# Performance work log

Hardware: AMD Instinct MI355X
Metric: run time of the kernel (lower is better)

Reference implementation:

```python
import jax, jax.numpy as jnp
import numpy as np

B, T, C = 2, 2048, 1024
NH, HS = 16, 64  # n_heads, head_size; NH*HS == C


def setup_inputs() -> dict:
    key = jax.random.key(0)
    k1, k2, k3 = jax.random.split(key, 3)
    x = jax.random.normal(k1, (B, T, C), dtype=jnp.float32)
    W_attn = jax.random.normal(k2, (C, 3 * C), dtype=jnp.float32) * (C ** -0.5)
    b_attn = jax.random.normal(k3, (3 * C,), dtype=jnp.float32) * 0.02
    return {"x": x, "W_attn": W_attn, "b_attn": b_attn}


def reference(x, W_attn, b_attn):
    Bv, Tv, Cv = x.shape
    qkv = x @ W_attn + b_attn                       # [B,T,3C]
    q, k, v = jnp.split(qkv, 3, axis=-1)            # each [B,T,C]
    q = q.reshape(Bv, Tv, NH, HS)
    k = k.reshape(Bv, Tv, NH, HS)
    v = v.reshape(Bv, Tv, NH, HS)
    scale = HS ** -0.5
    wei = jnp.einsum('bqhd,bkhd->bhqk', q, k) * scale  # [B,H,T,T]
    causal = jnp.tril(jnp.ones((Tv, Tv), dtype=bool))
    wei = jnp.where(causal[None, None], wei, -jnp.inf)
    wei = jax.nn.softmax(wei, axis=-1)
    # dropout layers are identity in eval mode
    out = jnp.einsum('bhqk,bkhd->bqhd', wei, v)     # [B,T,H,HS]
    return out.reshape(Bv, Tv, Cv)
```

## Files before the change

### kernel.cpp

```cpp
#include <hip/hip_runtime.h>
#include <hip/hip_bf16.h>
#include <math.h>

#define BB   2
#define TT   2048
#define CC   1024
#define NH   16
#define HS   64
#define N3C  3072
#define MM   4096

typedef __attribute__((ext_vector_type(8))) short bf16x8;
typedef __attribute__((ext_vector_type(4))) float f32x4;

#define NINF (-__builtin_inff())
#define QSCALE 0.125f

__device__ __forceinline__ unsigned short f2bf(float f) {
    unsigned int u = __builtin_bit_cast(unsigned int, f);
    unsigned int r = u + 0x7fffu + ((u >> 16) & 1u);
    return (unsigned short)(r >> 16);
}

__device__ __forceinline__ unsigned short f2bf_fast(float f) {
    unsigned int u = __builtin_bit_cast(unsigned int, f);
    return (unsigned short)((u + 0x8000u) >> 16);
}

__device__ __forceinline__ void gl_lds16(const unsigned short* g, unsigned short* l) {
    __builtin_amdgcn_global_load_lds(
        (const __attribute__((address_space(1))) unsigned int*)g,
        (__attribute__((address_space(3))) unsigned int*)l, 16, 0, 0);
}

__global__ __launch_bounds__(256) void k_cast(const float* __restrict__ x,
                                              unsigned short* __restrict__ xb) {
    int i = (blockIdx.x * 256 + threadIdx.x) * 4;
    float4 v = *(const float4*)(x + i);
    ushort4 o;
    o.x = f2bf(v.x); o.y = f2bf(v.y); o.z = f2bf(v.z); o.w = f2bf(v.w);
    *(ushort4*)(xb + i) = o;
}

__global__ __launch_bounds__(256) void k_transpose_w(const float* __restrict__ W,
                                                     unsigned short* __restrict__ Wt) {
    __shared__ float tile[32][33];
    const int n0 = blockIdx.x * 32;
    const int k0 = blockIdx.y * 32;
    const int t = threadIdx.x;
    {
        int kr = t >> 3, ns = (t & 7) * 4;
        float4 v = *(const float4*)(W + (size_t)(k0 + kr) * N3C + n0 + ns);
        tile[kr][ns + 0] = v.x; tile[kr][ns + 1] = v.y;
        tile[kr][ns + 2] = v.z; tile[kr][ns + 3] = v.w;
    }
    __syncthreads();
    {
        int nr = t >> 3, ks = (t & 7) * 4;
        ushort4 o;
        o.x = f2bf(tile[ks + 0][nr]);
        o.y = f2bf(tile[ks + 1][nr]);
        o.z = f2bf(tile[ks + 2][nr]);
        o.w = f2bf(tile[ks + 3][nr]);
        *(ushort4*)(Wt + (size_t)(n0 + nr) * CC + k0 + ks) = o;
    }
}

#define EPS 72

__global__ __launch_bounds__(256) void k_gemm_qkv(const unsigned short* __restrict__ xb,
                                                  const unsigned short* __restrict__ wt,
                                                  const float* __restrict__ bias,
                                                  unsigned short* __restrict__ qb,
                                                  unsigned short* __restrict__ kb,
                                                  unsigned short* __restrict__ vt) {
    __shared__ unsigned short sA[128 * 32];
    __shared__ unsigned short sB[128 * 32];
    __shared__ unsigned short sE[4 * 64 * EPS];
    const int t = threadIdx.x;
    const int wave = t >> 6, lane = t & 63;
    const int quad = lane >> 4, c16 = lane & 15;
    const int wm = wave >> 1, wn = wave & 1;
    const int m0 = blockIdx.y * 128;
    const int n0 = blockIdx.x * 128;
    const int sel = n0 >> 10;

    f32x4 acc[4][4];
#pragma unroll
    for (int i = 0; i < 4; ++i)
#pragma unroll
        for (int j = 0; j < 4; ++j) acc[i][j] = f32x4{0, 0, 0, 0};

    const int srow = wave * 16 + (lane >> 2);
    const int scol = (lane & 3) * 8;
    const unsigned short* gA = xb + (size_t)(m0 + srow) * CC + scol;
    const unsigned short* gB = wt + (size_t)(n0 + srow) * CC + scol;
    unsigned short* lA = sA + wave * 512 + lane * 8;
    unsigned short* lB = sB + wave * 512 + lane * 8;

    for (int k0 = 0; k0 < CC; k0 += 32) {
        __syncthreads();
        gl_lds16(gA + k0, lA);
        gl_lds16(gA + k0 + (size_t)64 * CC, lA + 2048);
        gl_lds16(gB + k0, lB);
        gl_lds16(gB + k0 + (size_t)64 * CC, lB + 2048);
        __syncthreads();
        bf16x8 a[4], b[4];
#pragma unroll
        for (int rt = 0; rt < 4; ++rt)
            a[rt] = *(const bf16x8*)(sA + (wm * 64 + rt * 16 + c16) * 32 + quad * 8);
#pragma unroll
        for (int ct = 0; ct < 4; ++ct)
            b[ct] = *(const bf16x8*)(sB + (wn * 64 + ct * 16 + c16) * 32 + quad * 8);
#pragma unroll
        for (int rt = 0; rt < 4; ++rt)
#pragma unroll
            for (int ct = 0; ct < 4; ++ct)
                acc[rt][ct] = __builtin_amdgcn_mfma_f32_16x16x32_bf16(b[ct], a[rt], acc[rt][ct], 0, 0, 0);
    }

    const int head = ((n0 + wn * 64) >> 6) & 15;
    const int bh = (m0 >> 11) * NH + head;
    const int tbase = (m0 & 2047) + wm * 64;
    if (sel < 2) {
        unsigned short* dst = (sel == 0) ? qb : kb;
        const float sc = (sel == 0) ? QSCALE : 1.0f;
        unsigned short* ew = sE + wave * (64 * EPS);
#pragma unroll
        for (int ct = 0; ct < 4; ++ct) {
            const float4 bv4 = *(const float4*)(bias + n0 + wn * 64 + ct * 16 + quad * 4);
            const int d0 = ct * 16 + quad * 4;
#pragma unroll
            for (int rt = 0; rt < 4; ++rt) {
                ushort4 pk;
                pk.x = f2bf((acc[rt][ct][0] + bv4.x) * sc);
                pk.y = f2bf((acc[rt][ct][1] + bv4.y) * sc);
                pk.z = f2bf((acc[rt][ct][2] + bv4.z) * sc);
                pk.w = f2bf((acc[rt][ct][3] + bv4.w) * sc);
                *(ushort4*)(ew + (rt * 16 + c16) * EPS + d0) = pk;
            }
        }
        const size_t gbase = ((size_t)bh * TT + tbase) * HS;
#pragma unroll
        for (int i = 0; i < 8; ++i) {
            const int trow = i * 8 + (lane >> 3);
            bf16x8 row = *(const bf16x8*)(ew + trow * EPS + (lane & 7) * 8);
            *(bf16x8*)(dst + gbase + (size_t)trow * HS + (lane & 7) * 8) = row;
        }
    } else {
#pragma unroll
        for (int ct = 0; ct < 4; ++ct) {
            const float4 bv4 = *(const float4*)(bias + n0 + wn * 64 + ct * 16 + quad * 4);
#pragma unroll
            for (int r = 0; r < 4; ++r) {
                const int d = ct * 16 + quad * 4 + r;
                const float bv = ((const float*)&bv4)[r];
#pragma unroll
                for (int rt = 0; rt < 4; ++rt) {
                    const int tt = tbase + rt * 16 + c16;
                    vt[((size_t)bh * HS + d) * TT + tt] = f2bf(acc[rt][ct][r] + bv);
                }
            }
        }
    }
}

#define SPP 72
#define AW  4

__global__ __launch_bounds__(256) void k_attn(const unsigned short* __restrict__ qb,
                                              const unsigned short* __restrict__ kb,
                                              const unsigned short* __restrict__ vt,
                                              float* __restrict__ out) {
    __shared__ unsigned short sK[2][64 * 64];
    __shared__ unsigned short sV[2][64 * 64];
    __shared__ unsigned short sP[AW][32 * SPP];

    const int tid = threadIdx.x;
    const int wave = tid >> 6, lane = tid & 63;
    const int quad = lane >> 4, c16 = lane & 15;
    const int g = blockIdx.x >> 5;
    const int qbk = 15 - g;
    const int bh = blockIdx.x & 31;
    const int qw = qbk * 128 + wave * 32;
    const int qmax = qw + 31;
    const int kiters = 2 * (qbk + 1);

    const unsigned short* Qp = qb + (size_t)bh * TT * HS;
    const unsigned short* Kp = kb + (size_t)bh * TT * HS;
    const unsigned short* Vp = vt + (size_t)bh * HS * TT;

    bf16x8 qf[2][2];
#pragma unroll
    for (int j = 0; j < 2; ++j)
#pragma unroll
        for (int ks = 0; ks < 2; ++ks)
            qf[j][ks] = *(const bf16x8*)(Qp + (size_t)(qw + j * 16 + c16) * HS + ks * 32 + quad * 8);

    f32x4 o[4][2];
#pragma unroll
    for (int dt = 0; dt < 4; ++dt)
#pragma unroll
        for (int j = 0; j < 2; ++j) o[dt][j] = f32x4{0, 0, 0, 0};
    float lsum[2] = {0.f, 0.f};

    unsigned short* sPw = sP[wave];

    const int srow = tid >> 3;
    const int ssc = tid & 7;
    auto stage = [&](int buf, int kt) {
        const int kb0 = kt * 64;
#pragma unroll
        for (int rnd = 0; rnd < 2; ++rnd) {
            const int row = rnd * 32 + srow;
            const int sl = ((ssc ^ (row & 7)) * 8);
            gl_lds16(Kp + (size_t)(kb0 + row) * HS + sl, &sK[buf][rnd * 2048 + tid * 8]);
            gl_lds16(Vp + (size_t)row * TT + kb0 + sl, &sV[buf][rnd * 2048 + tid * 8]);
        }
    };

    auto tile = [&](int buf, int kt) {
        const int kb0 = kt * 64;
        const unsigned short* Kb = sK[buf];
        const unsigned short* Vb = sV[buf];
        bf16x8 kf[4][2];
#pragma unroll
        for (int mt = 0; mt < 4; ++mt)
#pragma unroll
            for (int ks = 0; ks < 2; ++ks)
                kf[mt][ks] = *(const bf16x8*)(Kb + (mt * 16 + c16) * 64 +
                                              (((ks * 4 + quad) ^ (c16 & 7)) * 8));
        f32x4 s[4][2];
#pragma unroll
        for (int mt = 0; mt < 4; ++mt)
#pragma unroll
            for (int j = 0; j < 2; ++j) s[mt][j] = f32x4{0, 0, 0, 0};
#pragma unroll
        for (int mt = 0; mt < 4; ++mt)
#pragma unroll
            for (int j = 0; j < 2; ++j) {
                s[mt][j] = __builtin_amdgcn_mfma_f32_16x16x32_bf16(kf[mt][0], qf[j][0], s[mt][j], 0, 0, 0);
                s[mt][j] = __builtin_amdgcn_mfma_f32_16x16x32_bf16(kf[mt][1], qf[j][1], s[mt][j], 0, 0, 0);
            }
        bf16x8 vf[4][2];
#pragma unroll
        for (int dt = 0; dt < 4; ++dt)
#pragma unroll
            for (int ks = 0; ks < 2; ++ks)
                vf[dt][ks] = *(const bf16x8*)(Vb + (dt * 16 + c16) * 64 +
                                              (((ks * 4 + quad) ^ (c16 & 7)) * 8));
        const bool maskit = (kb0 + 63 > qw);
#pragma unroll
        for (int j = 0; j < 2; ++j) {
            const int rowq = qw + j * 16 + c16;
            float l = 0.f;
#pragma unroll
            for (int mt = 0; mt < 4; ++mt) {
                float p0, p1, p2, p3;
                if (maskit) {
                    const int k = kb0 + mt * 16 + quad * 4;
                    p0 = __expf((k     <= rowq) ? s[mt][j][0] : NINF);
                    p1 = __expf((k + 1 <= rowq) ? s[mt][j][1] : NINF);
                    p2 = __expf((k + 2 <= rowq) ? s[mt][j][2] : NINF);
                    p3 = __expf((k + 3 <= rowq) ? s[mt][j][3] : NINF);
                } else {
                    p0 = __expf(s[mt][j][0]);
                    p1 = __expf(s[mt][j][1]);
                    p2 = __expf(s[mt][j][2]);
                    p3 = __expf(s[mt][j][3]);
                }
                l += (p0 + p1) + (p2 + p3);
                ushort4 pk;
                pk.x = f2bf_fast(p0); pk.y = f2bf_fast(p1);
                pk.z = f2bf_fast(p2); pk.w = f2bf_fast(p3);
                *(ushort4*)(sPw + (j * 16 + c16) * SPP + mt * 16 + quad * 4) = pk;
            }
            lsum[j] += l;
        }
        bf16x8 pf[2][2];
#pragma unroll
        for (int j = 0; j < 2; ++j)
#pragma unroll
            for (int ks = 0; ks < 2; ++ks)
                pf[j][ks] = *(const bf16x8*)(sPw + (j * 16 + c16) * SPP + ks * 32 + quad * 8);
#pragma unroll
        for (int dt = 0; dt < 4; ++dt)
#pragma unroll
            for (int j = 0; j < 2; ++j) {
                o[dt][j] = __builtin_amdgcn_mfma_f32_16x16x32_bf16(vf[dt][0], pf[j][0], o[dt][j], 0, 0, 0);
                o[dt][j] = __builtin_amdgcn_mfma_f32_16x16x32_bf16(vf[dt][1], pf[j][1], o[dt][j], 0, 0, 0);
            }
    };

    stage(0, 0);
    for (int kt = 0; kt < kiters; ++kt) {
        if (kt + 1 < kiters) {
            stage((kt + 1) & 1, kt + 1);
            asm volatile("s_waitcnt vmcnt(4)" ::: "memory");
        } else {
            asm volatile("s_waitcnt vmcnt(0)" ::: "memory");
        }
        __builtin_amdgcn_s_barrier();
        asm volatile("" ::: "memory");
        if (kt * 64 <= qmax) tile(kt & 1, kt);
        __builtin_amdgcn_s_barrier();
        asm volatile("" ::: "memory");
    }

#pragma unroll
    for (int j = 0; j < 2; ++j) {
        lsum[j] += __shfl_xor(lsum[j], 16);
        lsum[j] += __shfl_xor(lsum[j], 32);
    }

    const int b_ = bh >> 4, h_ = bh & 15;
#pragma unroll
    for (int j = 0; j < 2; ++j) {
        const float il = 1.0f / lsum[j];
        const int q = qw + j * 16 + c16;
        float* orow = out + ((size_t)(b_ * TT + q)) * CC + h_ * HS;
#pragma unroll
        for (int dt = 0; dt < 4; ++dt) {
            float4 w;
            w.x = o[dt][j][0] * il; w.y = o[dt][j][1] * il;
            w.z = o[dt][j][2] * il; w.w = o[dt][j][3] * il;
            *(float4*)(orow + dt * 16 + quad * 4) = w;
        }
    }
}

extern "C" void kernel_launch(void* const* d_in, const int* in_sizes, int n_in,
                              void* d_out, int out_size, void* d_ws, size_t ws_size,
                              hipStream_t stream) {
    const float* x    = (const float*)d_in[0];
    const float* W    = (const float*)d_in[1];
    const float* bias = (const float*)d_in[2];
    float* out = (float*)d_out;

    char* ws = (char*)d_ws;
    unsigned short* xb = (unsigned short*)(ws);
    unsigned short* wt = (unsigned short*)(ws + 8388608);
    unsigned short* qb = (unsigned short*)(ws + 8388608 + 6291456);
    unsigned short* kb = (unsigned short*)(ws + 8388608 + 6291456 + 8388608);
    unsigned short* vt = (unsigned short*)(ws + 8388608 + 6291456 + 2 * 8388608);

    k_cast<<<dim3(MM * CC / (256 * 4)), dim3(256), 0, stream>>>(x, xb);
    k_transpose_w<<<dim3(N3C / 32, CC / 32), dim3(256), 0, stream>>>(W, wt);
    k_gemm_qkv<<<dim3(N3C / 128, MM / 128), dim3(256), 0, stream>>>(xb, wt, bias, qb, kb, vt);
    k_attn<<<dim3(16 * 32), dim3(256), 0, stream>>>(qb, kb, vt, out);
}
```

Baseline: 179.2 us.

## Pair causal query blocks in attention, widen GEMM K-tile, stage V transpose via LDS

```diff
diff --git a/kernel.cpp b/kernel.cpp
--- a/kernel.cpp
+++ b/kernel.cpp
@@ -74,9 +74,11 @@
                                                   unsigned short* __restrict__ qb,
                                                   unsigned short* __restrict__ kb,
                                                   unsigned short* __restrict__ vt) {
-    __shared__ unsigned short sA[128 * 32];
-    __shared__ unsigned short sB[128 * 32];
-    __shared__ unsigned short sE[4 * 64 * EPS];
+    __shared__ unsigned short smem[4 * 64 * EPS];
+    unsigned short* sA = smem;
+    unsigned short* sB = smem + 128 * 64;
+    unsigned short* sE = smem;
+
     const int t = threadIdx.x;
     const int wave = t >> 6, lane = t & 63;
     const int quad = lane >> 4, c16 = lane & 15;
@@ -91,33 +93,38 @@
 #pragma unroll
         for (int j = 0; j < 4; ++j) acc[i][j] = f32x4{0, 0, 0, 0};
 
-    const int srow = wave * 16 + (lane >> 2);
-    const int scol = (lane & 3) * 8;
-    const unsigned short* gA = xb + (size_t)(m0 + srow) * CC + scol;
-    const unsigned short* gB = wt + (size_t)(n0 + srow) * CC + scol;
-    unsigned short* lA = sA + wave * 512 + lane * 8;
-    unsigned short* lB = sB + wave * 512 + lane * 8;
-
-    for (int k0 = 0; k0 < CC; k0 += 32) {
+    const int srow_ = t >> 3;
+    const int sslot = t & 7;
+
+    for (int k0 = 0; k0 < CC; k0 += 64) {
         __syncthreads();
-        gl_lds16(gA + k0, lA);
-        gl_lds16(gA + k0 + (size_t)64 * CC, lA + 2048);
-        gl_lds16(gB + k0, lB);
-        gl_lds16(gB + k0 + (size_t)64 * CC, lB + 2048);
+#pragma unroll
+        for (int rnd = 0; rnd < 4; ++rnd) {
+            const int row = rnd * 32 + srow_;
+            const int sl = (sslot ^ (row & 7)) * 8;
+            gl_lds16(xb + (size_t)(m0 + row) * CC + k0 + sl, sA + rnd * 2048 + t * 8);
+            gl_lds16(wt + (size_t)(n0 + row) * CC + k0 + sl, sB + rnd * 2048 + t * 8);
+        }
         __syncthreads();
-        bf16x8 a[4], b[4];
-#pragma unroll
-        for (int rt = 0; rt < 4; ++rt)
-            a[rt] = *(const bf16x8*)(sA + (wm * 64 + rt * 16 + c16) * 32 + quad * 8);
-#pragma unroll
-        for (int ct = 0; ct < 4; ++ct)
-            b[ct] = *(const bf16x8*)(sB + (wn * 64 + ct * 16 + c16) * 32 + quad * 8);
-#pragma unroll
-        for (int rt = 0; rt < 4; ++rt)
+#pragma unroll
+        for (int ks = 0; ks < 2; ++ks) {
+            bf16x8 a[4], b[4];
+#pragma unroll
+            for (int rt = 0; rt < 4; ++rt)
+                a[rt] = *(const bf16x8*)(sA + (wm * 64 + rt * 16 + c16) * 64 +
+                                         (((ks * 4 + quad) ^ (c16 & 7)) * 8));
 #pragma unroll
             for (int ct = 0; ct < 4; ++ct)
-                acc[rt][ct] = __builtin_amdgcn_mfma_f32_16x16x32_bf16(b[ct], a[rt], acc[rt][ct], 0, 0, 0);
-    }
+                b[ct] = *(const bf16x8*)(sB + (wn * 64 + ct * 16 + c16) * 64 +
+                                         (((ks * 4 + quad) ^ (c16 & 7)) * 8));
+#pragma unroll
+            for (int rt = 0; rt < 4; ++rt)
+#pragma unroll
+                for (int ct = 0; ct < 4; ++ct)
+                    acc[rt][ct] = __builtin_amdgcn_mfma_f32_16x16x32_bf16(b[ct], a[rt], acc[rt][ct], 0, 0, 0);
+        }
+    }
+    __syncthreads();
 
     const int head = ((n0 + wn * 64) >> 6) & 15;
     const int bh = (m0 >> 11) * NH + head;
@@ -148,6 +155,7 @@
             *(bf16x8*)(dst + gbase + (size_t)trow * HS + (lane & 7) * 8) = row;
         }
     } else {
+        unsigned short* ew = sE + wave * (64 * EPS);
 #pragma unroll
         for (int ct = 0; ct < 4; ++ct) {
             const float4 bv4 = *(const float4*)(bias + n0 + wn * 64 + ct * 16 + quad * 4);
@@ -156,40 +164,46 @@
                 const int d = ct * 16 + quad * 4 + r;
                 const float bv = ((const float*)&bv4)[r];
 #pragma unroll
-                for (int rt = 0; rt < 4; ++rt) {
-                    const int tt = tbase + rt * 16 + c16;
-                    vt[((size_t)bh * HS + d) * TT + tt] = f2bf(acc[rt][ct][r] + bv);
-                }
-            }
+                for (int rt = 0; rt < 4; ++rt)
+                    ew[d * EPS + rt * 16 + c16] = f2bf(acc[rt][ct][r] + bv);
+            }
+        }
+        const size_t vbase = (size_t)bh * HS * TT + tbase;
+#pragma unroll
+        for (int i = 0; i < 8; ++i) {
+            const int d = i * 8 + (lane >> 3);
+            bf16x8 row = *(const bf16x8*)(ew + d * EPS + (lane & 7) * 8);
+            *(bf16x8*)(vt + vbase + (size_t)d * TT + (lane & 7) * 8) = row;
         }
     }
 }
 
 #define SPP 72
-#define AW  4
-
-__global__ __launch_bounds__(256) void k_attn(const unsigned short* __restrict__ qb,
+
+__global__ __launch_bounds__(512) void k_attn(const unsigned short* __restrict__ qb,
                                               const unsigned short* __restrict__ kb,
                                               const unsigned short* __restrict__ vt,
                                               float* __restrict__ out) {
     __shared__ unsigned short sK[2][64 * 64];
     __shared__ unsigned short sV[2][64 * 64];
-    __shared__ unsigned short sP[AW][32 * SPP];
+    __shared__ unsigned short sP[8][16 * SPP];
 
     const int tid = threadIdx.x;
     const int wave = tid >> 6, lane = tid & 63;
     const int quad = lane >> 4, c16 = lane & 15;
     const int g = blockIdx.x >> 5;
-    const int qbk = 15 - g;
     const int bh = blockIdx.x & 31;
-    const int qw = qbk * 128 + wave * 32;
+    const int p = (wave < 4) ? (15 - g) : g;
+    const int qw = p * 128 + (wave & 3) * 32;
     const int qmax = qw + 31;
-    const int kiters = 2 * (qbk + 1);
+    const int kiters = 32 - 2 * g;
 
     const unsigned short* Qp = qb + (size_t)bh * TT * HS;
     const unsigned short* Kp = kb + (size_t)bh * TT * HS;
     const unsigned short* Vp = vt + (size_t)bh * HS * TT;
 
+    unsigned short* sPw = sP[wave];
+
     bf16x8 qf[2][2];
 #pragma unroll
     for (int j = 0; j < 2; ++j)
@@ -204,19 +218,15 @@
         for (int j = 0; j < 2; ++j) o[dt][j] = f32x4{0, 0, 0, 0};
     float lsum[2] = {0.f, 0.f};
 
-    unsigned short* sPw = sP[wave];
-
     const int srow = tid >> 3;
     const int ssc = tid & 7;
+    const int sl = (ssc ^ (srow & 7)) * 8;
+    const unsigned short* Ksrc = Kp + (size_t)srow * HS + sl;
+    const unsigned short* Vsrc = Vp + (size_t)srow * TT + sl;
     auto stage = [&](int buf, int kt) {
         const int kb0 = kt * 64;
-#pragma unroll
-        for (int rnd = 0; rnd < 2; ++rnd) {
-            const int row = rnd * 32 + srow;
-            const int sl = ((ssc ^ (row & 7)) * 8);
-            gl_lds16(Kp + (size_t)(kb0 + row) * HS + sl, &sK[buf][rnd * 2048 + tid * 8]);
-            gl_lds16(Vp + (size_t)row * TT + kb0 + sl, &sV[buf][rnd * 2048 + tid * 8]);
-        }
+        gl_lds16(Ksrc + (size_t)kb0 * HS, &sK[buf][tid * 8]);
+        gl_lds16(Vsrc + kb0, &sV[buf][tid * 8]);
     };
 
     auto tile = [&](int buf, int kt) {
@@ -250,6 +260,7 @@
                 vf[dt][ks] = *(const bf16x8*)(Vb + (dt * 16 + c16) * 64 +
                                               (((ks * 4 + quad) ^ (c16 & 7)) * 8));
         const bool maskit = (kb0 + 63 > qw);
+        bf16x8 pf[2][2];
 #pragma unroll
         for (int j = 0; j < 2; ++j) {
             const int rowq = qw + j * 16 + c16;
@@ -273,16 +284,13 @@
                 ushort4 pk;
                 pk.x = f2bf_fast(p0); pk.y = f2bf_fast(p1);
                 pk.z = f2bf_fast(p2); pk.w = f2bf_fast(p3);
-                *(ushort4*)(sPw + (j * 16 + c16) * SPP + mt * 16 + quad * 4) = pk;
+                *(ushort4*)(sPw + c16 * SPP + mt * 16 + quad * 4) = pk;
             }
             lsum[j] += l;
-        }
-        bf16x8 pf[2][2];
-#pragma unroll
-        for (int j = 0; j < 2; ++j)
 #pragma unroll
             for (int ks = 0; ks < 2; ++ks)
-                pf[j][ks] = *(const bf16x8*)(sPw + (j * 16 + c16) * SPP + ks * 32 + quad * 8);
+                pf[j][ks] = *(const bf16x8*)(sPw + c16 * SPP + ks * 32 + quad * 8);
+        }
 #pragma unroll
         for (int dt = 0; dt < 4; ++dt)
 #pragma unroll
@@ -296,7 +304,7 @@
     for (int kt = 0; kt < kiters; ++kt) {
         if (kt + 1 < kiters) {
             stage((kt + 1) & 1, kt + 1);
-            asm volatile("s_waitcnt vmcnt(4)" ::: "memory");
+            asm volatile("s_waitcnt vmcnt(2)" ::: "memory");
         } else {
             asm volatile("s_waitcnt vmcnt(0)" ::: "memory");
         }
@@ -347,5 +355,5 @@
     k_cast<<<dim3(MM * CC / (256 * 4)), dim3(256), 0, stream>>>(x, xb);
     k_transpose_w<<<dim3(N3C / 32, CC / 32), dim3(256), 0, stream>>>(W, wt);
     k_gemm_qkv<<<dim3(N3C / 128, MM / 128), dim3(256), 0, stream>>>(xb, wt, bias, qb, kb, vt);
-    k_attn<<<dim3(16 * 32), dim3(256), 0, stream>>>(qb, kb, vt, out);
-}
+    k_attn<<<dim3(8 * 32), dim3(512), 0, stream>>>(qb, kb, vt, out);
+}
```

After: 169.6 us. -5.4%, faster.
